# Performance work log

Hardware: AMD Instinct MI355X
Metric: run time of the kernel (lower is better)

Reference implementation:

```python
import jax, jax.numpy as jnp
import numpy as np

N, D, H = 96, 64, 256  # num_nodes, input_dim, hidden_dim


def setup_inputs() -> dict:
    key = jax.random.key(0)
    ks = jax.random.split(key, 12)

    def lin(k, fan_in, fan_out):
        return jax.random.normal(k, (fan_in, fan_out), jnp.float32) / np.sqrt(fan_in)

    return {
        "node_features": jax.random.normal(ks[0], (N, D), jnp.float32),
        "edge_index": jax.random.randint(ks[1], (2, 1536), 0, N),
        # causal_discovery MLP: Linear(2D,H) -> ReLU -> Linear(H,H//2) -> ReLU -> Linear(H//2,1) -> Sigmoid
        "W1": lin(ks[2], 2 * D, H),      "b1": jnp.zeros((H,), jnp.float32),
        "W2": lin(ks[3], H, H // 2),     "b2": jnp.zeros((H // 2,), jnp.float32),
        "W3": lin(ks[4], H // 2, 1),     "b3": jnp.zeros((1,), jnp.float32),
        # confounder_detector MLP: Linear(3D,H) -> ReLU -> Linear(H,1) -> Sigmoid
        "V1": lin(ks[5], 3 * D, H),      "c1": jnp.zeros((H,), jnp.float32),
        "V2": lin(ks[6], H, 1),          "c2": jnp.zeros((1,), jnp.float32),
    }


def reference(node_features, edge_index, W1, b1, W2, b2, W3, b3, V1, c1, V2, c2):
    n, d = node_features.shape
    eye = jnp.eye(n, dtype=bool)

    # ---- discover_causal_structure: all ordered pairs (i, j), i != j ----
    # Linear on concat([x_i, x_j]) == x_i @ W1[:d] + x_j @ W1[d:] + b1
    pi = node_features @ W1[:d]           # [N, H]
    pj = node_features @ W1[d:]           # [N, H]
    h = jax.nn.relu(pi[:, None, :] + pj[None, :, :] + b1)   # [N, N, H]
    h = jax.nn.relu(h @ W2 + b2)                             # [N, N, H//2]
    causal = jax.nn.sigmoid((h @ W3 + b3)[..., 0])           # [N, N]
    causal = jnp.where(eye, 0.0, causal)                     # diagonal stays zero

    # ---- detect_confounders: all distinct triplets (i, j, k) ----
    ta = node_features @ V1[:d]            # [N, H]
    tb = node_features @ V1[d:2 * d]       # [N, H]
    tc = node_features @ V1[2 * d:]        # [N, H]
    t = jax.nn.relu(ta[:, None, None, :] + tb[None, :, None, :]
                    + tc[None, None, :, :] + c1)             # [N, N, N, H]
    conf = jax.nn.sigmoid((t @ V2 + c2)[..., 0])             # [N, N, N]
    distinct = (~eye[:, :, None]) & (~eye[None, :, :]) & (~eye[:, None, :])
    conf = jnp.where(distinct, conf, 0.0)

    return causal, conf
```

## Files before the change

kernel.cpp:

```cpp
#include <hip/hip_runtime.h>
#include <hip/hip_bf16.h>

#define NN 96
#define DD 64
#define HH 256
#define H2 128

typedef float v2f __attribute__((ext_vector_type(2)));

__global__ __launch_bounds__(256) void proj_kernel(
    const float* __restrict__ X, const float* __restrict__ W1, const float* __restrict__ b1,
    const float* __restrict__ V1, const float* __restrict__ c1,
    float* __restrict__ pi, float* __restrict__ pj,
    float* __restrict__ ta, float* __restrict__ tb, float* __restrict__ tcP)
{
    const int i = blockIdx.x;
    const int h = threadIdx.x;
    __shared__ float xs[DD];
    if (h < DD) xs[h] = X[i*DD + h];
    __syncthreads();
    float aPi = 0.f, aPj = 0.f, aTa = 0.f, aTb = 0.f, aTc = 0.f;
    #pragma unroll 8
    for (int d = 0; d < DD; ++d) {
        const float x = xs[d];
        aPi = fmaf(x, W1[d*HH + h],          aPi);
        aPj = fmaf(x, W1[(DD + d)*HH + h],   aPj);
        aTa = fmaf(x, V1[d*HH + h],          aTa);
        aTb = fmaf(x, V1[(DD + d)*HH + h],   aTb);
        aTc = fmaf(x, V1[(2*DD + d)*HH + h], aTc);
    }
    pi[i*HH + h] = aPi + b1[h];
    pj[i*HH + h] = aPj;
    ta[i*HH + h] = aTa + c1[h];
    tb[i*HH + h] = aTb;
    tcP[((h >> 1)*NN + i)*2 + (h & 1)] = aTc;
}

__global__ __launch_bounds__(256) void fused_kernel(
    const float* __restrict__ pi, const float* __restrict__ pj,
    const float* __restrict__ W2, const float* __restrict__ b2,
    const float* __restrict__ W3, const float* __restrict__ b3,
    const float* __restrict__ ta, const float* __restrict__ tb,
    const float* __restrict__ tcP, const float* __restrict__ V2,
    const float* __restrict__ c2, float* __restrict__ out)
{
    __shared__ float smem[4*64*2*12 + 2*12];
    const int i  = blockIdx.x;
    const int by = blockIdx.y;
    const int t  = threadIdx.x;

    if (by < 8) {
        const int j0 = by * 12;
        const int c2c = t & 63;
        const int qt  = t >> 6;

        float (*hb)[12]          = (float(*)[12])smem;
        float (*part)[64][2][12] = (float(*)[64][2][12])smem;
        float (*red)[12]         = (float(*)[12])(smem + 6144);

        {
            const float p_i = pi[i*HH + t];
            #pragma unroll
            for (int jj = 0; jj < 12; ++jj)
                hb[t][jj] = fmaxf(p_i + pj[(j0 + jj)*HH + t], 0.f);
        }
        __syncthreads();

        v2f acc0[6], acc1[6];
        #pragma unroll
        for (int p = 0; p < 6; ++p) { acc0[p] = (v2f)(0.f); acc1[p] = (v2f)(0.f); }

        const float* __restrict__ w2p = W2 + (qt*64)*H2 + c2c;
        #pragma unroll 2
        for (int q = 0; q < 64; ++q) {
            const float wa = w2p[q*H2];
            const float wb = w2p[q*H2 + 64];
            const v2f wa2 = {wa, wa};
            const v2f wb2 = {wb, wb};
            const int hq = qt*64 + q;
            const float4 hA = *(const float4*)&hb[hq][0];
            const float4 hB = *(const float4*)&hb[hq][4];
            const float4 hC = *(const float4*)&hb[hq][8];
            const v2f hp[6] = {{hA.x,hA.y},{hA.z,hA.w},
                               {hB.x,hB.y},{hB.z,hB.w},
                               {hC.x,hC.y},{hC.z,hC.w}};
            #pragma unroll
            for (int p = 0; p < 6; ++p) {
                acc0[p] += hp[p] * wa2;
                acc1[p] += hp[p] * wb2;
            }
        }
        __syncthreads();

        #pragma unroll
        for (int b = 0; b < 3; ++b) {
            float4 p0, p1;
            p0.x = acc0[b*2].x; p0.y = acc0[b*2].y; p0.z = acc0[b*2+1].x; p0.w = acc0[b*2+1].y;
            p1.x = acc1[b*2].x; p1.y = acc1[b*2].y; p1.z = acc1[b*2+1].x; p1.w = acc1[b*2+1].y;
            *(float4*)&part[qt][c2c][0][b*4] = p0;
            *(float4*)&part[qt][c2c][1][b*4] = p1;
        }
        __syncthreads();

        if (t < 128) {
            const int cl = t & 63;
            const int cc = t >> 6;
            const float b2c = b2[t];
            const float w3c = W3[t];
            float v[12];
            #pragma unroll
            for (int b = 0; b < 3; ++b) {
                float4 s; s.x = 0.f; s.y = 0.f; s.z = 0.f; s.w = 0.f;
                #pragma unroll
                for (int qq = 0; qq < 4; ++qq) {
                    const float4 p = *(const float4*)&part[qq][cl][cc][b*4];
                    s.x += p.x; s.y += p.y; s.z += p.z; s.w += p.w;
                }
                v[b*4+0] = fmaxf(s.x + b2c, 0.f) * w3c;
                v[b*4+1] = fmaxf(s.y + b2c, 0.f) * w3c;
                v[b*4+2] = fmaxf(s.z + b2c, 0.f) * w3c;
                v[b*4+3] = fmaxf(s.w + b2c, 0.f) * w3c;
            }
            #pragma unroll
            for (int jj = 0; jj < 12; ++jj) {
                float s = v[jj];
                #pragma unroll
                for (int off = 32; off; off >>= 1) s += __shfl_down(s, off, 64);
                if ((t & 63) == 0) red[t >> 6][jj] = s;
            }
        }
        __syncthreads();
        if (t < 12) {
            const int j = j0 + t;
            const float s = red[0][t] + red[1][t] + b3[0];
            out[i*NN + j] = (i == j) ? 0.f : 1.f / (1.f + __expf(-s));
        }
    } else {
        const int j0 = (by - 8) * 24;
        float (*sbuf)[HH] = (float(*)[HH])smem;
        float* outc = out + NN*NN;

        for (int idx = t; idx < 24*HH/4; idx += 256) {
            const int jj = idx >> 6;
            const int h4 = (idx & 63) << 2;
            const float4 a = *(const float4*)&ta[i*HH + h4];
            const float4 b = *(const float4*)&tb[(j0 + jj)*HH + h4];
            float4 s; s.x = a.x + b.x; s.y = a.y + b.y; s.z = a.z + b.z; s.w = a.w + b.w;
            *(float4*)&sbuf[jj][h4] = s;
        }
        __syncthreads();

        if (t < 192) {
            const int jg = t / 24;
            const int l  = t % 24;
            const int k0 = 4*l;

            v2f acc[3][4];
            #pragma unroll
            for (int m = 0; m < 3; ++m)
                #pragma unroll
                for (int x = 0; x < 4; ++x) acc[m][x] = (v2f)(0.f);

            const float* __restrict__ sb0 = &sbuf[jg*3 + 0][0];
            const float* __restrict__ sb1 = &sbuf[jg*3 + 1][0];
            const float* __restrict__ sb2 = &sbuf[jg*3 + 2][0];
            const v2f vzero = (v2f)(0.f);

            #pragma unroll 2
            for (int h0 = 0; h0 < HH; h0 += 4) {
                const int hp = h0 >> 1;
                const float4 tA0 = *(const float4*)&tcP[(hp*NN + k0)*2];
                const float4 tA1 = *(const float4*)&tcP[(hp*NN + k0 + 2)*2];
                const float4 tB0 = *(const float4*)&tcP[((hp+1)*NN + k0)*2];
                const float4 tB1 = *(const float4*)&tcP[((hp+1)*NN + k0 + 2)*2];
                const float4 vv = *(const float4*)&V2[h0];
                const float4 sA = *(const float4*)&sb0[h0];
                const float4 sB = *(const float4*)&sb1[h0];
                const float4 sC = *(const float4*)&sb2[h0];
                const v2f va01 = {vv.x, vv.y}, va23 = {vv.z, vv.w};
                const v2f tka[4] = {{tA0.x,tA0.y},{tA0.z,tA0.w},
                                    {tA1.x,tA1.y},{tA1.z,tA1.w}};
                const v2f tkb[4] = {{tB0.x,tB0.y},{tB0.z,tB0.w},
                                    {tB1.x,tB1.y},{tB1.z,tB1.w}};
                const v2f sp[3][2] = {{{sA.x,sA.y},{sA.z,sA.w}},
                                      {{sB.x,sB.y},{sB.z,sB.w}},
                                      {{sC.x,sC.y},{sC.z,sC.w}}};
                #pragma unroll
                for (int m = 0; m < 3; ++m) {
                    #pragma unroll
                    for (int kk = 0; kk < 4; ++kk) {
                        v2f x;
                        x = __builtin_elementwise_max(sp[m][0] + tka[kk], vzero);
                        acc[m][kk] += x * va01;
                        x = __builtin_elementwise_max(sp[m][1] + tkb[kk], vzero);
                        acc[m][kk] += x * va23;
                    }
                }
            }

            const float c2v = c2[0];
            #pragma unroll
            for (int m = 0; m < 3; ++m) {
                const int j = j0 + jg*3 + m;
                float4 o;
                o.x = 1.f / (1.f + __expf(-(acc[m][0].x + acc[m][0].y + c2v)));
                o.y = 1.f / (1.f + __expf(-(acc[m][1].x + acc[m][1].y + c2v)));
                o.z = 1.f / (1.f + __expf(-(acc[m][2].x + acc[m][2].y + c2v)));
                o.w = 1.f / (1.f + __expf(-(acc[m][3].x + acc[m][3].y + c2v)));
                if (i == j || i == k0   || j == k0  ) o.x = 0.f;
                if (i == j || i == k0+1 || j == k0+1) o.y = 0.f;
                if (i == j || i == k0+2 || j == k0+2) o.z = 0.f;
                if (i == j || i == k0+3 || j == k0+3) o.w = 0.f;
                *(float4*)&outc[(i*NN + j)*NN + k0] = o;
            }
        }
    }
}

extern "C" void kernel_launch(void* const* d_in, const int* in_sizes, int n_in,
                              void* d_out, int out_size, void* d_ws, size_t ws_size,
                              hipStream_t stream) {
    const float* X  = (const float*)d_in[0];
    const float* W1 = (const float*)d_in[2];
    const float* b1 = (const float*)d_in[3];
    const float* W2 = (const float*)d_in[4];
    const float* b2 = (const float*)d_in[5];
    const float* W3 = (const float*)d_in[6];
    const float* b3 = (const float*)d_in[7];
    const float* V1 = (const float*)d_in[8];
    const float* c1 = (const float*)d_in[9];
    const float* V2 = (const float*)d_in[10];
    const float* c2 = (const float*)d_in[11];

    float* out = (float*)d_out;
    float* ws  = (float*)d_ws;
    float* pi  = ws;
    float* pj  = pi + NN*HH;
    float* ta  = pj + NN*HH;
    float* tb  = ta + NN*HH;
    float* tcP = tb + NN*HH;

    proj_kernel<<<NN, 256, 0, stream>>>(X, W1, b1, V1, c1, pi, pj, ta, tb, tcP);
    fused_kernel<<<dim3(NN, 12), 256, 0, stream>>>(pi, pj, W2, b2, W3, b3,
                                                   ta, tb, tcP, V2, c2, out);
}
```

Baseline: 49.45 us.

## Split confounder hidden dimension across thread pairs and double confounder blocks

The confounder branch now gives each block 12 j rows instead of 24, and the grid grows from 12 to 16 blocks in y. Each pair of threads splits the 256-wide hidden reduction into two halves and combines them with a lane shuffle. The shared buffer is padded to 260 floats so the two halves fall on different LDS banks. The aim is more blocks and shorter per-thread loops for better occupancy and latency hiding, at the cost of extra shuffles and half the threads idling during the output write.

```diff
diff --git a/kernel.cpp b/kernel.cpp
--- a/kernel.cpp
+++ b/kernel.cpp
@@ -136,23 +136,25 @@
             out[i*NN + j] = (i == j) ? 0.f : 1.f / (1.f + __expf(-s));
         }
     } else {
-        const int j0 = (by - 8) * 24;
-        float (*sbuf)[HH] = (float(*)[HH])smem;
+        const int j0 = (by - 8) * 12;
+        float (*sbuf)[260] = (float(*)[260])smem;
         float* outc = out + NN*NN;
 
-        for (int idx = t; idx < 24*HH/4; idx += 256) {
+        for (int idx = t; idx < 12*64; idx += 256) {
             const int jj = idx >> 6;
             const int h4 = (idx & 63) << 2;
             const float4 a = *(const float4*)&ta[i*HH + h4];
             const float4 b = *(const float4*)&tb[(j0 + jj)*HH + h4];
             float4 s; s.x = a.x + b.x; s.y = a.y + b.y; s.z = a.z + b.z; s.w = a.w + b.w;
-            *(float4*)&sbuf[jj][h4] = s;
+            *(float4*)&sbuf[jj][h4 + ((h4 >> 7) << 2)] = s;
         }
         __syncthreads();
 
         if (t < 192) {
-            const int jg = t / 24;
-            const int l  = t % 24;
+            const int hh = t & 1;
+            const int pr = t >> 1;
+            const int g  = pr / 24;
+            const int l  = pr % 24;
             const int k0 = 4*l;
 
             v2f acc[3][4];
@@ -161,19 +163,21 @@
                 #pragma unroll
                 for (int x = 0; x < 4; ++x) acc[m][x] = (v2f)(0.f);
 
-            const float* __restrict__ sb0 = &sbuf[jg*3 + 0][0];
-            const float* __restrict__ sb1 = &sbuf[jg*3 + 1][0];
-            const float* __restrict__ sb2 = &sbuf[jg*3 + 2][0];
+            const float* __restrict__ sb0 = &sbuf[g*3 + 0][hh*132];
+            const float* __restrict__ sb1 = &sbuf[g*3 + 1][hh*132];
+            const float* __restrict__ sb2 = &sbuf[g*3 + 2][hh*132];
+            const float* __restrict__ tp  = tcP + (hh*64)*NN*2;
+            const float* __restrict__ vp  = V2 + hh*128;
             const v2f vzero = (v2f)(0.f);
 
             #pragma unroll 2
-            for (int h0 = 0; h0 < HH; h0 += 4) {
+            for (int h0 = 0; h0 < 128; h0 += 4) {
                 const int hp = h0 >> 1;
-                const float4 tA0 = *(const float4*)&tcP[(hp*NN + k0)*2];
-                const float4 tA1 = *(const float4*)&tcP[(hp*NN + k0 + 2)*2];
-                const float4 tB0 = *(const float4*)&tcP[((hp+1)*NN + k0)*2];
-                const float4 tB1 = *(const float4*)&tcP[((hp+1)*NN + k0 + 2)*2];
-                const float4 vv = *(const float4*)&V2[h0];
+                const float4 tA0 = *(const float4*)&tp[(hp*NN + k0)*2];
+                const float4 tA1 = *(const float4*)&tp[(hp*NN + k0 + 2)*2];
+                const float4 tB0 = *(const float4*)&tp[((hp+1)*NN + k0)*2];
+                const float4 tB1 = *(const float4*)&tp[((hp+1)*NN + k0 + 2)*2];
+                const float4 vv = *(const float4*)&vp[h0];
                 const float4 sA = *(const float4*)&sb0[h0];
                 const float4 sB = *(const float4*)&sb1[h0];
                 const float4 sC = *(const float4*)&sb2[h0];
@@ -198,20 +202,30 @@
                 }
             }
 
-            const float c2v = c2[0];
-            #pragma unroll
-            for (int m = 0; m < 3; ++m) {
-                const int j = j0 + jg*3 + m;
-                float4 o;
-                o.x = 1.f / (1.f + __expf(-(acc[m][0].x + acc[m][0].y + c2v)));
-                o.y = 1.f / (1.f + __expf(-(acc[m][1].x + acc[m][1].y + c2v)));
-                o.z = 1.f / (1.f + __expf(-(acc[m][2].x + acc[m][2].y + c2v)));
-                o.w = 1.f / (1.f + __expf(-(acc[m][3].x + acc[m][3].y + c2v)));
-                if (i == j || i == k0   || j == k0  ) o.x = 0.f;
-                if (i == j || i == k0+1 || j == k0+1) o.y = 0.f;
-                if (i == j || i == k0+2 || j == k0+2) o.z = 0.f;
-                if (i == j || i == k0+3 || j == k0+3) o.w = 0.f;
-                *(float4*)&outc[(i*NN + j)*NN + k0] = o;
+            #pragma unroll
+            for (int m = 0; m < 3; ++m)
+                #pragma unroll
+                for (int kk = 0; kk < 4; ++kk) {
+                    acc[m][kk].x += __shfl_xor(acc[m][kk].x, 1, 64);
+                    acc[m][kk].y += __shfl_xor(acc[m][kk].y, 1, 64);
+                }
+
+            if (hh == 0) {
+                const float c2v = c2[0];
+                #pragma unroll
+                for (int m = 0; m < 3; ++m) {
+                    const int j = j0 + g*3 + m;
+                    float4 o;
+                    o.x = 1.f / (1.f + __expf(-(acc[m][0].x + acc[m][0].y + c2v)));
+                    o.y = 1.f / (1.f + __expf(-(acc[m][1].x + acc[m][1].y + c2v)));
+                    o.z = 1.f / (1.f + __expf(-(acc[m][2].x + acc[m][2].y + c2v)));
+                    o.w = 1.f / (1.f + __expf(-(acc[m][3].x + acc[m][3].y + c2v)));
+                    if (i == j || i == k0   || j == k0  ) o.x = 0.f;
+                    if (i == j || i == k0+1 || j == k0+1) o.y = 0.f;
+                    if (i == j || i == k0+2 || j == k0+2) o.z = 0.f;
+                    if (i == j || i == k0+3 || j == k0+3) o.w = 0.f;
+                    *(float4*)&outc[(i*NN + j)*NN + k0] = o;
+                }
             }
         }
     }
@@ -241,6 +255,6 @@
     float* tcP = tb + NN*HH;
 
     proj_kernel<<<NN, 256, 0, stream>>>(X, W1, b1, V1, c1, pi, pj, ta, tb, tcP);
-    fused_kernel<<<dim3(NN, 12), 256, 0, stream>>>(pi, pj, W2, b2, W3, b3,
+    fused_kernel<<<dim3(NN, 16), 256, 0, stream>>>(pi, pj, W2, b2, W3, b3,
                                                    ta, tb, tcP, V2, c2, out);
 }
```

New measurement: 48.55 us. No clear change (-1.8%).
